# Kernel tuning notes

Measured on AMD Instinct MI355X. Metric: run time of the kernel, lower is better.

Reference implementation:

```python
import jax, jax.numpy as jnp
import numpy as np

NUM_CLASSES = 172
IGNORE_INDEX = 255
DICE_WEIGHT = 0.5
EPS = 1e-7


def setup_inputs() -> dict:
    key = jax.random.key(0)
    k1, k2 = jax.random.split(key)
    pred = jax.random.normal(k1, (4, NUM_CLASSES, 256, 256), dtype=jnp.float32)
    target = jax.random.randint(k2, (4, 256, 256), 0, NUM_CLASSES, dtype=jnp.int32)
    return {"pred": pred, "target": target}


def reference(pred, target):
    # pred: [B, C, H, W] logits; target: [B, H, W] int labels (255 = ignore)
    C = NUM_CLASSES
    logp = jax.nn.log_softmax(pred, axis=1)  # [B, C, H, W]

    # ---- cross entropy with ignore_index (mean over valid pixels) ----
    valid = target != IGNORE_INDEX  # [B, H, W]
    safe_tgt = jnp.where(valid, target, 0)
    nll = -jnp.take_along_axis(logp, safe_tgt[:, None].astype(jnp.int32), axis=1)[:, 0]  # [B, H, W]
    n_valid = jnp.sum(valid)
    ce = jnp.sum(jnp.where(valid, nll, 0.0)) / jnp.maximum(n_valid, 1).astype(pred.dtype)

    # ---- dice loss: vectorized over classes (replaces per-class python loop) ----
    p = jnp.exp(logp)  # softmax probs [B, C, H, W]
    # intersection[c] = sum over pixels with target==c of p[:, c] at those pixels
    gathered = jnp.take_along_axis(p, safe_tgt[:, None].astype(jnp.int32), axis=1)[:, 0]  # [B, H, W]
    seg_ids = target.ravel().astype(jnp.int32)  # ignore pixels land in bucket 255, discarded
    inter = jax.ops.segment_sum(gathered.ravel(), seg_ids, num_segments=256)[:C]  # [C]
    counts = jax.ops.segment_sum(jnp.ones_like(gathered.ravel()), seg_ids, num_segments=256)[:C]
    union = jnp.sum(p, axis=(0, 2, 3)) + counts  # [C]
    valid_c = union > 0
    dice_terms = jnp.where(valid_c, (2.0 * inter + EPS) / (union + EPS), 0.0)
    n_valid_c = jnp.sum(valid_c).astype(pred.dtype)
    dice = jnp.where(n_valid_c > 0, 1.0 - jnp.sum(dice_terms) / jnp.maximum(n_valid_c, 1.0), 0.0)

    return ce + DICE_WEIGHT * dice
```

## Files before the change

kernel.cpp:

```cpp
#include <hip/hip_runtime.h>
#include <stdint.h>

#define NCLS 172
#define IGN 255
#define HW 65536
#define NPIX 262144
#define EPSV 1e-7f
#define TP 64
#define NTILE 4
#define PIXPERBLK (TP * NTILE)
#define NSTAGE 16
#define SS 520

__device__ __forceinline__ float waveReduceSum(float v) {
    #pragma unroll
    for (int off = 32; off > 0; off >>= 1) v += __shfl_down(v, off, 64);
    return v;
}

__device__ __forceinline__ void gl_lds16(const float* g, float* l) {
    __builtin_amdgcn_global_load_lds(
        (const __attribute__((address_space(1))) void*)g,
        (__attribute__((address_space(3))) void*)l, 16, 0, 0);
}

__global__ __launch_bounds__(256) void seg_fused(
    const float* __restrict__ pred, const int* __restrict__ tgt,
    float* __restrict__ part)
{
    __shared__ float tile[NCLS * TP];
    __shared__ float sPart[256];
    __shared__ float sInvs[TP];
    __shared__ float sInter[NCLS];
    __shared__ unsigned int sCnt[NCLS];

    const int tid  = threadIdx.x;
    const int lane = tid & 63;
    const int wv   = tid >> 6;
    const int p    = lane;
    const int q    = wv;

    for (int i = tid; i < NCLS; i += 256) { sInter[i] = 0.f; sCnt[i] = 0u; }

    const int pix0 = blockIdx.x * PIXPERBLK;
    const int b    = pix0 >> 16;
    const int hw0  = pix0 & (HW - 1);
    const float* gb = pred + (size_t)b * NCLS * HW + hw0;

    const int lc = lane >> 4;
    const int lp = (lane & 15) << 2;

    float unionAcc = 0.f;
    float ceAcc = 0.f, nvAcc = 0.f;

    for (int tI = 0; tI < NTILE; ++tI) {
        const float* gt = gb + tI * TP;
        for (int cb = wv * 4; cb < NCLS; cb += 16)
            gl_lds16(gt + (size_t)(cb + lc) * HW + lp, &tile[cb * TP]);
        __syncthreads();

        const int c0 = q * 43;
        float s0 = 0.f, s1 = 0.f;
        #pragma unroll
        for (int i = 0; i < 42; i += 2) {
            s0 += __expf(tile[(c0 + i    ) * TP + p]);
            s1 += __expf(tile[(c0 + i + 1) * TP + p]);
        }
        s0 += __expf(tile[(c0 + 42) * TP + p]);
        sPart[tid] = s0 + s1;
        __syncthreads();

        if (tid < 64) {
            const float s    = (sPart[p] + sPart[64 + p]) + (sPart[128 + p] + sPart[192 + p]);
            const float invs = 1.0f / s;
            sInvs[p] = invs;
            const int  t     = tgt[pix0 + tI * TP + p];
            const bool valid = (t != IGN);
            const int  st    = valid ? t : 0;
            const float xt   = tile[st * TP + p];
            const float nll  = valid ? (__logf(s) - xt) : 0.f;
            if (valid) {
                atomicAdd(&sInter[st], __expf(xt) * invs);
                atomicAdd(&sCnt[st], 1u);
            }
            const float vr = waveReduceSum(nll);
            const float nr = waveReduceSum(valid ? 1.f : 0.f);
            if (lane == 0) { ceAcc += vr; nvAcc += nr; }
        }
        __syncthreads();

        if (tid < NCLS) {
            const int c = tid;
            float u0 = 0.f, u1 = 0.f;
            #pragma unroll 4
            for (int k = 0; k < TP; k += 2) {
                const int p0 = (c + k    ) & (TP - 1);
                const int p1 = (c + k + 1) & (TP - 1);
                u0 += __expf(tile[c * TP + p0]) * sInvs[p0];
                u1 += __expf(tile[c * TP + p1]) * sInvs[p1];
            }
            unionAcc += u0 + u1;
        }
        __syncthreads();
    }

    float* pb = part + (size_t)(blockIdx.x & (NSTAGE - 1)) * SS;
    for (int i = tid; i < NCLS; i += 256) {
        const float vi = sInter[i];
        if (vi != 0.f) atomicAdd(&pb[i], vi);
        const unsigned int ci = sCnt[i];
        if (ci != 0u) atomicAdd(&pb[NCLS + i], (float)ci);
    }
    if (tid < NCLS) atomicAdd(&pb[344 + tid], unionAcc);
    if (tid == 0) { atomicAdd(&pb[516], ceAcc); atomicAdd(&pb[517], nvAcc); }
}

__global__ __launch_bounds__(256) void seg_fin(
    const float* __restrict__ part, float* __restrict__ out)
{
    __shared__ float sT[256], sN[256];
    const int tid = threadIdx.x;
    float term = 0.f, nv = 0.f;
    if (tid < NCLS) {
        float inter = 0.f, cnt = 0.f, uni = 0.f;
        #pragma unroll
        for (int st = 0; st < NSTAGE; ++st) {
            inter += part[st * SS + tid];
            cnt   += part[st * SS + NCLS + tid];
            uni   += part[st * SS + 344 + tid];
        }
        const float u = uni + cnt;
        if (u > 0.f) { term = (2.f * inter + EPSV) / (u + EPSV); nv = 1.f; }
    }
    sT[tid] = term; sN[tid] = nv;
    __syncthreads();
    #pragma unroll
    for (int s2 = 128; s2 > 0; s2 >>= 1) {
        if (tid < s2) { sT[tid] += sT[tid + s2]; sN[tid] += sN[tid + s2]; }
        __syncthreads();
    }
    if (tid == 0) {
        float ce = 0.f, nvl = 0.f;
        #pragma unroll
        for (int st = 0; st < NSTAGE; ++st) {
            ce  += part[st * SS + 516];
            nvl += part[st * SS + 517];
        }
        const float ceo  = ce / fmaxf(nvl, 1.f);
        const float dice = (sN[0] > 0.f) ? (1.f - sT[0] / fmaxf(sN[0], 1.f)) : 0.f;
        out[0] = ceo + 0.5f * dice;
    }
}

extern "C" void kernel_launch(void* const* d_in, const int* in_sizes, int n_in,
                              void* d_out, int out_size, void* d_ws, size_t ws_size,
                              hipStream_t stream) {
    const float* pred = (const float*)d_in[0];
    const int*   tgt  = (const int*)d_in[1];
    float* out  = (float*)d_out;
    float* part = (float*)d_ws;

    hipMemsetAsync(d_ws, 0, NSTAGE * SS * sizeof(float), stream);
    seg_fused<<<NPIX / PIXPERBLK, 256, 0, stream>>>(pred, tgt, part);
    seg_fin<<<1, 256, 0, stream>>>(part, out);
}
```

Measured before the change: 260.1 us.

## Halve pixel tile, cache exponentials in LDS, and double partial-sum stages

The pixel tile shrinks from 64 to 32 pixels, so the grid doubles to 2048 blocks and each block uses less LDS, which may allow more resident blocks. The exp pass now writes exp(x) back into the tile, so the target-gather and union passes reuse it instead of recomputing exp. The NLL becomes -log(p_t), computed from the cached value. NSTAGE doubles to spread the global atomic contention. The costs are an extra LDS write pass, more blocks doing global atomics, and clamped padding loads for the tile rows beyond 172.

```diff
diff --git a/kernel.cpp b/kernel.cpp
--- a/kernel.cpp
+++ b/kernel.cpp
@@ -6,17 +6,12 @@
 #define HW 65536
 #define NPIX 262144
 #define EPSV 1e-7f
-#define TP 64
+#define TP 32
+#define TROWS 176
 #define NTILE 4
 #define PIXPERBLK (TP * NTILE)
-#define NSTAGE 16
+#define NSTAGE 32
 #define SS 520
-
-__device__ __forceinline__ float waveReduceSum(float v) {
-    #pragma unroll
-    for (int off = 32; off > 0; off >>= 1) v += __shfl_down(v, off, 64);
-    return v;
-}
 
 __device__ __forceinline__ void gl_lds16(const float* g, float* l) {
     __builtin_amdgcn_global_load_lds(
@@ -28,17 +23,17 @@
     const float* __restrict__ pred, const int* __restrict__ tgt,
     float* __restrict__ part)
 {
-    __shared__ float tile[NCLS * TP];
-    __shared__ float sPart[256];
+    __shared__ float tile[TROWS * TP];
+    __shared__ float sPart[128];
     __shared__ float sInvs[TP];
     __shared__ float sInter[NCLS];
     __shared__ unsigned int sCnt[NCLS];
 
-    const int tid  = threadIdx.x;
-    const int lane = tid & 63;
-    const int wv   = tid >> 6;
-    const int p    = lane;
-    const int q    = wv;
+    const int tid   = threadIdx.x;
+    const int lane  = tid & 63;
+    const int wv    = tid >> 6;
+    const int p     = tid & 31;
+    const int chunk = tid >> 5;
 
     for (int i = tid; i < NCLS; i += 256) { sInter[i] = 0.f; sCnt[i] = 0u; }
 
@@ -47,57 +42,73 @@
     const int hw0  = pix0 & (HW - 1);
     const float* gb = pred + (size_t)b * NCLS * HW + hw0;
 
-    const int lc = lane >> 4;
-    const int lp = (lane & 15) << 2;
+    const int scb = lane >> 3;
+    const int spo = (lane & 7) << 2;
 
     float unionAcc = 0.f;
     float ceAcc = 0.f, nvAcc = 0.f;
 
     for (int tI = 0; tI < NTILE; ++tI) {
         const float* gt = gb + tI * TP;
-        for (int cb = wv * 4; cb < NCLS; cb += 16)
-            gl_lds16(gt + (size_t)(cb + lc) * HW + lp, &tile[cb * TP]);
+
+        for (int ib = wv; ib < 22; ib += 4) {
+            int cb = ib * 8 + scb;
+            if (cb > NCLS - 1) cb = NCLS - 1;
+            gl_lds16(gt + (size_t)cb * HW + spo, &tile[ib * (8 * TP)]);
+        }
         __syncthreads();
 
-        const int c0 = q * 43;
         float s0 = 0.f, s1 = 0.f;
         #pragma unroll
-        for (int i = 0; i < 42; i += 2) {
-            s0 += __expf(tile[(c0 + i    ) * TP + p]);
-            s1 += __expf(tile[(c0 + i + 1) * TP + p]);
+        for (int k = 0; k < 20; k += 2) {
+            const int i0 = (chunk + 8 * k) * TP + p;
+            const int i1 = (chunk + 8 * k + 8) * TP + p;
+            const float e0 = __expf(tile[i0]);
+            const float e1 = __expf(tile[i1]);
+            tile[i0] = e0; tile[i1] = e1;
+            s0 += e0; s1 += e1;
         }
-        s0 += __expf(tile[(c0 + 42) * TP + p]);
-        sPart[tid] = s0 + s1;
+        {   const int i0 = (chunk + 160) * TP + p;
+            const float e = __expf(tile[i0]); tile[i0] = e; s0 += e; }
+        if (chunk < 4) {
+            const int i1 = (chunk + 168) * TP + p;
+            const float e = __expf(tile[i1]); tile[i1] = e; s1 += e;
+        }
+        float sv = s0 + s1;
+        sv += __shfl_down(sv, 32, 64);
+        if (lane < 32) sPart[wv * 32 + p] = sv;
         __syncthreads();
 
-        if (tid < 64) {
-            const float s    = (sPart[p] + sPart[64 + p]) + (sPart[128 + p] + sPart[192 + p]);
+        if (tid < 32) {
+            const float s    = (sPart[p] + sPart[32 + p]) + (sPart[64 + p] + sPart[96 + p]);
             const float invs = 1.0f / s;
             sInvs[p] = invs;
             const int  t     = tgt[pix0 + tI * TP + p];
             const bool valid = (t != IGN);
             const int  st    = valid ? t : 0;
-            const float xt   = tile[st * TP + p];
-            const float nll  = valid ? (__logf(s) - xt) : 0.f;
-            if (valid) {
-                atomicAdd(&sInter[st], __expf(xt) * invs);
-                atomicAdd(&sCnt[st], 1u);
+            const float et   = tile[st * TP + p];
+            const float pt   = et * invs;
+            float nll = valid ? -__logf(pt) : 0.f;
+            float nv  = valid ? 1.f : 0.f;
+            if (valid) { atomicAdd(&sInter[st], pt); atomicAdd(&sCnt[st], 1u); }
+            #pragma unroll
+            for (int off = 16; off > 0; off >>= 1) {
+                nll += __shfl_down(nll, off, 64);
+                nv  += __shfl_down(nv,  off, 64);
             }
-            const float vr = waveReduceSum(nll);
-            const float nr = waveReduceSum(valid ? 1.f : 0.f);
-            if (lane == 0) { ceAcc += vr; nvAcc += nr; }
+            if (tid == 0) { ceAcc += nll; nvAcc += nv; }
         }
         __syncthreads();
 
         if (tid < NCLS) {
-            const int c = tid;
+            const float* tr = &tile[tid * TP];
             float u0 = 0.f, u1 = 0.f;
-            #pragma unroll 4
+            #pragma unroll
             for (int k = 0; k < TP; k += 2) {
-                const int p0 = (c + k    ) & (TP - 1);
-                const int p1 = (c + k + 1) & (TP - 1);
-                u0 += __expf(tile[c * TP + p0]) * sInvs[p0];
-                u1 += __expf(tile[c * TP + p1]) * sInvs[p1];
+                const int p0 = (tid + k)     & (TP - 1);
+                const int p1 = (tid + k + 1) & (TP - 1);
+                u0 += tr[p0] * sInvs[p0];
+                u1 += tr[p1] * sInvs[p1];
             }
             unionAcc += u0 + u1;
         }
@@ -123,7 +134,6 @@
     float term = 0.f, nv = 0.f;
     if (tid < NCLS) {
         float inter = 0.f, cnt = 0.f, uni = 0.f;
-        #pragma unroll
         for (int st = 0; st < NSTAGE; ++st) {
             inter += part[st * SS + tid];
             cnt   += part[st * SS + NCLS + tid];
@@ -141,7 +151,6 @@
     }
     if (tid == 0) {
         float ce = 0.f, nvl = 0.f;
-        #pragma unroll
         for (int st = 0; st < NSTAGE; ++st) {
             ce  += part[st * SS + 516];
             nvl += part[st * SS + 517];
```

After: 255.3 us. No clear change (-1.8%).
